# Kernel optimization log

Hardware: AMD Instinct MI355X
Metric: run time of the kernel (lower is better)

The kernel has to match this reference:

```python
import jax, jax.numpy as jnp
import numpy as np

DESIRED_SIZE = 512.0
STRIDE = DESIRED_SIZE / 16.0  # Constants.desired_size / 16
EPS = 1e-7
IOU_SCALE = 2.0
DIOU_SCALE = 0.5
SL1_SCALE = 1.0
GOOD_MULT = 2.0
BAD_MULT = 1.5


def setup_inputs() -> dict:
    key = jax.random.key(0)
    k1, k2 = jax.random.split(key)
    pred_boxes = jax.random.normal(k1, (64, 3, 32, 32, 5), dtype=jnp.float32)
    # uniform in [0, desired_size); every row has positive sum => all boxes valid,
    # so filter_and_trim keeps exactly max_boxes=100 per batch (fixed-k topk)
    target_boxes = jax.random.uniform(k2, (64, 100, 4), dtype=jnp.float32) * DESIRED_SIZE
    return {"pred_boxes": pred_boxes, "target_boxes": target_boxes}


def _postprocess(pred):
    # pred: [B, A, H, W, 5] -> absolute (x, y, w, h), conf
    B, A, H, W, _ = pred.shape
    cx = jnp.arange(W, dtype=pred.dtype)[None, None, None, :]
    cy = jnp.arange(H, dtype=pred.dtype)[None, None, :, None]
    x = (jax.nn.sigmoid(pred[..., 0]) + cx) * STRIDE
    y = (jax.nn.sigmoid(pred[..., 1]) + cy) * STRIDE
    wh = jnp.exp(pred[..., 2:4]) * STRIDE
    conf = jax.nn.sigmoid(pred[..., 4])
    return jnp.stack([x, y, wh[..., 0], wh[..., 1]], axis=-1), conf


def _fix_box_coordinates(b, epsilon=1.0):
    x1 = jnp.minimum(b[..., 0], b[..., 2])
    y1 = jnp.minimum(b[..., 1], b[..., 3])
    x2 = jnp.maximum(b[..., 0], b[..., 2])
    y2 = jnp.maximum(b[..., 1], b[..., 3])
    x2 = jnp.where(x1 == x2, x1 + epsilon, x2)
    y2 = jnp.where(y1 == y2, y1 + epsilon, y2)
    return jnp.stack([x1, y1, x2, y2], axis=-1)


def _yolo_to_corners(b):
    xc, yc, w, h = b[..., 0], b[..., 1], b[..., 2], b[..., 3]
    return jnp.stack([xc - w / 2, yc - h / 2, xc + w / 2, yc + h / 2], axis=-1)


def _box_iou(a, b):
    # torchvision.ops.box_iou: a [N,4], b [M,4] -> [N,M]
    area_a = (a[:, 2] - a[:, 0]) * (a[:, 3] - a[:, 1])
    area_b = (b[:, 2] - b[:, 0]) * (b[:, 3] - b[:, 1])
    lt = jnp.maximum(a[:, None, :2], b[None, :, :2])
    rb = jnp.minimum(a[:, None, 2:], b[None, :, 2:])
    wh = jnp.clip(rb - lt, 0.0)
    inter = wh[..., 0] * wh[..., 1]
    return inter / (area_a[:, None] + area_b[None, :] - inter)


def _diou_loss(p, t, eps=EPS):
    pa = jnp.clip(p[..., 2] - p[..., 0], 0.0) * jnp.clip(p[..., 3] - p[..., 1], 0.0)
    ta = jnp.clip(t[..., 2] - t[..., 0], 0.0) * jnp.clip(t[..., 3] - t[..., 1], 0.0)
    ix1 = jnp.maximum(p[..., 0], t[..., 0]); iy1 = jnp.maximum(p[..., 1], t[..., 1])
    ix2 = jnp.minimum(p[..., 2], t[..., 2]); iy2 = jnp.minimum(p[..., 3], t[..., 3])
    inter = jnp.clip(ix2 - ix1, 0.0) * jnp.clip(iy2 - iy1, 0.0)
    iou = inter / (pa + ta - inter + eps)
    pcx = (p[..., 0] + p[..., 2]) / 2; pcy = (p[..., 1] + p[..., 3]) / 2
    tcx = (t[..., 0] + t[..., 2]) / 2; tcy = (t[..., 1] + t[..., 3]) / 2
    cdist = (pcx - tcx) ** 2 + (pcy - tcy) ** 2
    ex1 = jnp.minimum(p[..., 0], t[..., 0]); ey1 = jnp.minimum(p[..., 1], t[..., 1])
    ex2 = jnp.maximum(p[..., 2], t[..., 2]); ey2 = jnp.maximum(p[..., 3], t[..., 3])
    diag = (ex2 - ex1) ** 2 + (ey2 - ey1) ** 2
    return 1.0 - (iou - cdist / (diag + eps))


def _smooth_l1_mean(p, t):
    d = p - t
    ad = jnp.abs(d)
    return jnp.mean(jnp.where(ad < 1.0, 0.5 * d * d, ad - 0.5))


def reference(pred_boxes, target_boxes):
    # negative-size penalty computed on RAW (pre-postprocess) width/height
    pw = pred_boxes[..., 2]
    ph = pred_boxes[..., 3]
    neg_pen = (jnp.clip(1.0 - pw, 0.0) + jnp.clip(1.0 - ph, 0.0)).mean()

    coords, conf = _postprocess(pred_boxes)
    B = pred_boxes.shape[0]
    coords = coords.reshape(B, -1, 4)   # [B, A*H*W, 4]
    conf = conf.reshape(B, -1)          # [B, A*H*W]

    K = target_boxes.shape[1]  # all targets valid by construction -> fixed k
    topv, topi = jax.lax.top_k(conf, K)                      # [B, K]
    pred_sel = jnp.take_along_axis(coords, topi[..., None], axis=1)  # [B, K, 4]

    target_flat = target_boxes.reshape(-1, 4)   # [N, 4], N = B*K
    pred_flat = pred_sel.reshape(-1, 4)
    conf_flat = topv.reshape(-1, 1)             # [N, 1]

    target_c = _fix_box_coordinates(target_flat)
    pred_c = _yolo_to_corners(pred_flat)

    # IoULoss: max over preds of full NxN IoU matrix, per target
    iou_mat = _box_iou(pred_c, target_c)
    max_iou = jnp.clip(jnp.nan_to_num(jnp.max(iou_mat, axis=0)), 0.0)
    iou_loss = 1.0 - max_iou                    # [N]

    sl1 = _smooth_l1_mean(pred_c, target_c) / DESIRED_SIZE  # scalar
    diou = _diou_loss(pred_c, target_c)         # [N]

    max_loss = IOU_SCALE + DIOU_SCALE + SL1_SCALE  # 3.5
    # NOTE: source adds UNSCALED diou into x (faithful to original)
    x = iou_loss * IOU_SCALE + diou + sl1 * SL1_SCALE   # [N]
    y = conf_flat                                        # [N, 1] -> broadcast to [N, N]
    good = jnp.sqrt((0.0 - x) ** 2 + (1.0 - y) ** 2) * GOOD_MULT
    bad = jnp.sqrt((max_loss - x) ** 2 + (1.0 - y) ** 2) * BAD_MULT
    losses = jnp.clip(jnp.mean(good - bad) + max_loss * BAD_MULT, 0.0)
    return losses + neg_pen
```

## Files before the change

### kernel.cpp

```cpp
#include <hip/hip_runtime.h>
#include <cmath>

#define NKEY 3072
#define KSEL 100
#define PCHUNK 200

static __device__ __forceinline__ float sigf(float v) {
    return 1.0f / (1.0f + expf(-v));
}

static __device__ double block_reduce_sum(double v) {
    __shared__ double sh[4];
    __syncthreads();
    for (int off = 32; off > 0; off >>= 1) v += __shfl_down(v, off, 64);
    int lane = threadIdx.x & 63, wid = threadIdx.x >> 6;
    if (lane == 0) sh[wid] = v;
    __syncthreads();
    v = (threadIdx.x < 4) ? sh[threadIdx.x] : 0.0;
    if (wid == 0) {
        v += __shfl_down(v, 2, 64);
        v += __shfl_down(v, 1, 64);
    }
    return v;
}

__global__ __launch_bounds__(256) void k_topk(const float* __restrict__ pred,
                                              const float* __restrict__ tgt,
                                              float* __restrict__ predc,
                                              float* __restrict__ targc,
                                              float* __restrict__ confv,
                                              unsigned int* __restrict__ maxiou_bits,
                                              double* __restrict__ negp ,
                                              float* __restrict__ diouv,
                                              double* __restrict__ sl1p ,
                                              double* __restrict__ pair_sum,
                                              unsigned int* __restrict__ done_cnt) {
    const int b = blockIdx.x;
    const int t = threadIdx.x;

    __shared__ unsigned long long keys[NKEY];
    __shared__ unsigned int hist[256];
    __shared__ unsigned long long sel[KSEL];
    __shared__ float4 pbox[KSEL];
    __shared__ float4 tbox[KSEL];
    __shared__ unsigned long long tkey_sh;
    __shared__ unsigned int scnt;
    __shared__ int bdigit_sh;
    __shared__ int bk_sh;

    if (b == 0 && t == 0) { *pair_sum = 0.0; *done_cnt = 0u; }

    if (t < KSEL) {
        int n = b * KSEL + t;
        const float* tb = tgt + (size_t)n * 4;
        float a0 = tb[0], a1 = tb[1], a2 = tb[2], a3 = tb[3];
        float x1 = fminf(a0, a2), y1 = fminf(a1, a3);
        float x2 = fmaxf(a0, a2), y2 = fmaxf(a1, a3);
        if (x1 == x2) x2 = x1 + 1.0f;
        if (y1 == y2) y2 = y1 + 1.0f;
        targc[n * 4 + 0] = x1; targc[n * 4 + 1] = y1;
        targc[n * 4 + 2] = x2; targc[n * 4 + 3] = y2;
        tbox[t] = make_float4(x1, y1, x2, y2);
        maxiou_bits[n] = 0u;
    }
    if (t == 0) scnt = 0;

    const float* pb = pred + (size_t)b * (NKEY * 5);
    float negacc = 0.0f;
    for (int r = 0; r < 12; ++r) {
        int idx = t + r * 256;
        const float* pe = pb + (size_t)idx * 5;
        float w = pe[2], h = pe[3], cl = pe[4];
        negacc += fmaxf(1.0f - w, 0.0f) + fmaxf(1.0f - h, 0.0f);
        float c = sigf(cl);
        keys[idx] = ((unsigned long long)__float_as_uint(c) << 32)
                  | (unsigned long long)(0xFFFFFFFFu - (unsigned)idx);
    }
    {
        double v = block_reduce_sum((double)negacc);
        if (t == 0) negp[b] = v;
    }
    __syncthreads();

    unsigned long long prefix = 0ull;
    int plen = 0;
    int k = KSEL;
    bool done = false;
    for (int round = 0; round < 8 && !done; ++round) {
        hist[t] = 0u;
        __syncthreads();
        int shift = 56 - 8 * round;
        for (int r = 0; r < 12; ++r) {
            unsigned long long key = keys[t + r * 256];
            if (plen == 0 || (key >> (64 - plen)) == (prefix >> (64 - plen))) {
                atomicAdd(&hist[(unsigned)((key >> shift) & 0xFFull)], 1u);
            }
        }
        __syncthreads();
        if (t < 64) {
            unsigned s0 = hist[4 * t + 0], s1 = hist[4 * t + 1];
            unsigned s2 = hist[4 * t + 2], s3 = hist[4 * t + 3];
            unsigned ssum = s0 + s1 + s2 + s3;
            unsigned suf = ssum;
            for (int off = 1; off < 64; off <<= 1) {
                unsigned o = __shfl_down(suf, off, 64);
                if (t + off < 64) suf += o;
            }
            unsigned above = suf - ssum;
            if (above < (unsigned)k && suf >= (unsigned)k) {
                unsigned hh[4] = {s0, s1, s2, s3};
                unsigned cum = above;
                for (int q = 3; q >= 0; --q) {
                    unsigned c = hh[q];
                    if (cum + c >= (unsigned)k) { bdigit_sh = 4 * t + q; bk_sh = k - (int)cum; break; }
                    cum += c;
                }
            }
        }
        __syncthreads();
        int d = bdigit_sh;
        k = bk_sh;
        prefix |= ((unsigned long long)(unsigned)d) << shift;
        plen += 8;
        unsigned ceq = hist[d];
        if (ceq == 1u) {
            for (int r = 0; r < 12; ++r) {
                unsigned long long key = keys[t + r * 256];
                if ((key >> (64 - plen)) == (prefix >> (64 - plen))) tkey_sh = key;
            }
            done = true;
        }
        __syncthreads();
    }
    unsigned long long T = tkey_sh;

    for (int r = 0; r < 12; ++r) {
        unsigned long long key = keys[t + r * 256];
        if (key >= T) {
            unsigned pos = atomicAdd(&scnt, 1u);
            sel[pos] = key;
        }
    }
    __syncthreads();
    if (t < KSEL) {
        unsigned long long key = sel[t];
        int rank = 0;
        for (int p = 0; p < KSEL; ++p) rank += (sel[p] > key) ? 1 : 0;
        unsigned idx = 0xFFFFFFFFu - (unsigned)(key & 0xFFFFFFFFull);
        float conf = __uint_as_float((unsigned)(key >> 32));
        int n = b * KSEL + rank;
        confv[n] = conf;
        const float* pe = pb + (size_t)idx * 5;
        int w = idx & 31, h = (idx >> 5) & 31;
        float x  = (sigf(pe[0]) + (float)w) * 32.0f;
        float y  = (sigf(pe[1]) + (float)h) * 32.0f;
        float bw = expf(pe[2]) * 32.0f;
        float bh = expf(pe[3]) * 32.0f;
        float4 pc = make_float4(x - bw * 0.5f, y - bh * 0.5f,
                                x + bw * 0.5f, y + bh * 0.5f);
        predc[n * 4 + 0] = pc.x; predc[n * 4 + 1] = pc.y;
        predc[n * 4 + 2] = pc.z; predc[n * 4 + 3] = pc.w;
        pbox[rank] = pc;
    }
    __syncthreads();

    double s = 0.0;
    if (t < KSEL) {
        float4 p = pbox[t];
        float4 tj = tbox[t];
        float pa = fmaxf(p.z - p.x, 0.f) * fmaxf(p.w - p.y, 0.f);
        float ta2 = fmaxf(tj.z - tj.x, 0.f) * fmaxf(tj.w - tj.y, 0.f);
        float ix1 = fmaxf(p.x, tj.x), iy1 = fmaxf(p.y, tj.y);
        float ix2 = fminf(p.z, tj.z), iy2 = fminf(p.w, tj.w);
        float inter = fmaxf(ix2 - ix1, 0.f) * fmaxf(iy2 - iy1, 0.f);
        float iou = inter / (pa + ta2 - inter + 1e-7f);
        float pcx = (p.x + p.z) * 0.5f, pcy = (p.y + p.w) * 0.5f;
        float tcx = (tj.x + tj.z) * 0.5f, tcy = (tj.y + tj.w) * 0.5f;
        float cd = (pcx - tcx) * (pcx - tcx) + (pcy - tcy) * (pcy - tcy);
        float ex1 = fminf(p.x, tj.x), ey1 = fminf(p.y, tj.y);
        float ex2 = fmaxf(p.z, tj.z), ey2 = fmaxf(p.w, tj.w);
        float dg = (ex2 - ex1) * (ex2 - ex1) + (ey2 - ey1) * (ey2 - ey1);
        diouv[b * KSEL + t] = 1.0f - (iou - cd / (dg + 1e-7f));
        float d0 = p.x - tj.x, d1 = p.y - tj.y, d2 = p.z - tj.z, d3 = p.w - tj.w;
        float a0 = fabsf(d0), a1 = fabsf(d1), a2 = fabsf(d2), a3 = fabsf(d3);
        s += (double)(a0 < 1.f ? 0.5f * d0 * d0 : a0 - 0.5f);
        s += (double)(a1 < 1.f ? 0.5f * d1 * d1 : a1 - 0.5f);
        s += (double)(a2 < 1.f ? 0.5f * d2 * d2 : a2 - 0.5f);
        s += (double)(a3 < 1.f ? 0.5f * d3 * d3 : a3 - 0.5f);
    }
    double v = block_reduce_sum(s);
    if (t == 0) sl1p[b] = v;
}

__global__ __launch_bounds__(256) void k_maxiou(const float* __restrict__ predc,
                                                const float* __restrict__ targc,
                                                unsigned int* __restrict__ maxiou_bits) {
    __shared__ float4 pl[PCHUNK];
    __shared__ float pa_sh[PCHUNK];
    int t = threadIdx.x;
    int j = blockIdx.x * 256 + t;
    const float4* pc4 = (const float4*)predc;
    int i0 = blockIdx.y * PCHUNK;
    for (int i = t; i < PCHUNK; i += 256) {
        float4 p = pc4[i0 + i];
        pl[i] = p;
        pa_sh[i] = (p.z - p.x) * (p.w - p.y);
    }
    float4 tj = ((const float4*)targc)[j];
    float ta = (tj.z - tj.x) * (tj.w - tj.y);
    __syncthreads();
    float m0 = 0.0f, m1 = 0.0f;
    #pragma unroll 2
    for (int i = 0; i < PCHUNK; i += 2) {
        float4 p = pl[i];
        float w0 = fmaxf(fminf(p.z, tj.z) - fmaxf(p.x, tj.x), 0.0f);
        float h0 = fmaxf(fminf(p.w, tj.w) - fmaxf(p.y, tj.y), 0.0f);
        float in0 = w0 * h0;
        float iou0 = in0 * __builtin_amdgcn_rcpf(pa_sh[i] + ta - in0);
        m0 = fmaxf(m0, iou0);
        float4 q = pl[i + 1];
        float w1 = fmaxf(fminf(q.z, tj.z) - fmaxf(q.x, tj.x), 0.0f);
        float h1 = fmaxf(fminf(q.w, tj.w) - fmaxf(q.y, tj.y), 0.0f);
        float in1 = w1 * h1;
        float iou1 = in1 * __builtin_amdgcn_rcpf(pa_sh[i + 1] + ta - in1);
        m1 = fmaxf(m1, iou1);
    }
    m0 = fmaxf(m0, m1);
    atomicMax(&maxiou_bits[j], __float_as_uint(m0));
}

__global__ __launch_bounds__(256) void k_pair(const unsigned int* __restrict__ maxiou_bits,
                                              const float* __restrict__ diouv,
                                              const float* __restrict__ confv,
                                              const double* __restrict__ sl1p ,
                                              const double* __restrict__ negp,
                                              double* __restrict__ pair_sum,
                                              unsigned int* __restrict__ done_cnt,
                                              float* __restrict__ out) {
    __shared__ float oy2s[256];
    __shared__ float sl1_sh;
    int t = threadIdx.x;
    int j = blockIdx.x * 256 + t;
    if (t == 0) {
        double s = 0.0;
        for (int i = 0; i < 64; ++i) s += sl1p[i];
        sl1_sh = (float)(s / 25600.0 / 512.0);
    }
    {
        float oy = 1.0f - confv[blockIdx.y * 256 + t];
        oy2s[t] = oy * oy;
    }
    float mj = __uint_as_float(maxiou_bits[j]);
    float dj = diouv[j];
    __syncthreads();
    float xj = (1.0f - mj) * 2.0f + dj + sl1_sh;
    float a2 = xj * xj;
    float bb = 3.5f - xj;
    float b2 = bb * bb;
    float acc0 = 0.0f, acc1 = 0.0f;
    #pragma unroll 4
    for (int i = 0; i < 256; i += 2) {
        float o0 = oy2s[i], o1 = oy2s[i + 1];
        acc0 += 2.0f * __builtin_amdgcn_sqrtf(a2 + o0)
              - 1.5f * __builtin_amdgcn_sqrtf(b2 + o0);
        acc1 += 2.0f * __builtin_amdgcn_sqrtf(a2 + o1)
              - 1.5f * __builtin_amdgcn_sqrtf(b2 + o1);
    }
    double v = block_reduce_sum((double)(acc0 + acc1));
    if (t == 0) {
        atomicAdd(pair_sum, v);
        __threadfence();
        unsigned prev = atomicAdd(done_cnt, 1u);
        if (prev == 624u) {
            double ps = atomicAdd(pair_sum, 0.0);
            double ns = 0.0;
            for (int i = 0; i < 64; ++i) ns += negp[i];
            double mean_pair = ps / 40960000.0;
            float losses = fmaxf((float)mean_pair + 5.25f, 0.0f);
            float neg = (float)(ns / 196608.0);
            out[0] = losses + neg;
        }
    }
}


extern "C" void kernel_launch(void* const* d_in, const int* in_sizes, int n_in,
                              void* d_out, int out_size, void* d_ws, size_t ws_size,
                              hipStream_t stream) {
    const float* pred = (const float*)d_in[0];
    const float* tgt  = (const float*)d_in[1];
    float* out = (float*)d_out;

    char* ws = (char*)d_ws;
    double* negp     = (double*)ws;
    double* sl1p     = negp + 64;
    double* pair_sum = negp + 128;
    unsigned int* done_cnt = (unsigned int*)(negp + 129);
    float* fbase  = (float*)(ws + 6400);
    float* predc  = fbase;
    float* targc  = fbase + 25600;
    float* confv  = fbase + 51200;
    float* diouv  = fbase + 57600;
    unsigned int* maxiou_bits = (unsigned int*)(fbase + 64000);

    k_topk<<<64, 256, 0, stream>>>(pred, tgt, predc, targc, confv, maxiou_bits,
                                   negp, diouv, sl1p, pair_sum, done_cnt);
    k_maxiou<<<dim3(25, 32), 256, 0, stream>>>(predc, targc, maxiou_bits);
    k_pair<<<dim3(25, 25), 256, 0, stream>>>(maxiou_bits, diouv, confv, sl1p,
                                             negp, pair_sum, done_cnt, out);
}
```

Measured before the change: 115.8 us.

## Fuse three kernels into one persistent kernel with grid-wide barriers

```diff
diff --git a/kernel.cpp b/kernel.cpp
--- a/kernel.cpp
+++ b/kernel.cpp
@@ -4,6 +4,7 @@
 #define NKEY 3072
 #define KSEL 100
 #define PCHUNK 200
+#define NBLK 256
 
 static __device__ __forceinline__ float sigf(float v) {
     return 1.0f / (1.0f + expf(-v));
@@ -24,18 +25,26 @@
     return v;
 }
 
-__global__ __launch_bounds__(256) void k_topk(const float* __restrict__ pred,
-                                              const float* __restrict__ tgt,
-                                              float* __restrict__ predc,
-                                              float* __restrict__ targc,
-                                              float* __restrict__ confv,
-                                              unsigned int* __restrict__ maxiou_bits,
-                                              double* __restrict__ negp ,
-                                              float* __restrict__ diouv,
-                                              double* __restrict__ sl1p ,
-                                              double* __restrict__ pair_sum,
-                                              unsigned int* __restrict__ done_cnt) {
-    const int b = blockIdx.x;
+static __device__ void gsync(unsigned int* bar, unsigned int target) {
+    __syncthreads();
+    if (threadIdx.x == 0) {
+        __threadfence();
+        atomicAdd(bar, 1u);
+        while (atomicAdd(bar, 0u) < target) __builtin_amdgcn_s_sleep(8);
+        __threadfence();
+    }
+    __syncthreads();
+}
+
+__global__ __launch_bounds__(256) void k_fused(
+        const float* __restrict__ pred, const float* __restrict__ tgt,
+        float* __restrict__ predc, float* __restrict__ targc,
+        float* __restrict__ confv, unsigned int* __restrict__ maxiou_bits,
+        double* __restrict__ negp , float* __restrict__ diouv,
+        double* __restrict__ sl1p , unsigned int* __restrict__ bar,
+        double* __restrict__ pair_sum, unsigned int* __restrict__ done_cnt,
+        float* __restrict__ out) {
+    const int bid = blockIdx.x;
     const int t = threadIdx.x;
 
     __shared__ unsigned long long keys[NKEY];
@@ -47,231 +56,236 @@
     __shared__ unsigned int scnt;
     __shared__ int bdigit_sh;
     __shared__ int bk_sh;
-
-    if (b == 0 && t == 0) { *pair_sum = 0.0; *done_cnt = 0u; }
-
-    if (t < KSEL) {
-        int n = b * KSEL + t;
-        const float* tb = tgt + (size_t)n * 4;
-        float a0 = tb[0], a1 = tb[1], a2 = tb[2], a3 = tb[3];
-        float x1 = fminf(a0, a2), y1 = fminf(a1, a3);
-        float x2 = fmaxf(a0, a2), y2 = fmaxf(a1, a3);
-        if (x1 == x2) x2 = x1 + 1.0f;
-        if (y1 == y2) y2 = y1 + 1.0f;
-        targc[n * 4 + 0] = x1; targc[n * 4 + 1] = y1;
-        targc[n * 4 + 2] = x2; targc[n * 4 + 3] = y2;
-        tbox[t] = make_float4(x1, y1, x2, y2);
-        maxiou_bits[n] = 0u;
-    }
-    if (t == 0) scnt = 0;
-
-    const float* pb = pred + (size_t)b * (NKEY * 5);
-    float negacc = 0.0f;
-    for (int r = 0; r < 12; ++r) {
-        int idx = t + r * 256;
-        const float* pe = pb + (size_t)idx * 5;
-        float w = pe[2], h = pe[3], cl = pe[4];
-        negacc += fmaxf(1.0f - w, 0.0f) + fmaxf(1.0f - h, 0.0f);
-        float c = sigf(cl);
-        keys[idx] = ((unsigned long long)__float_as_uint(c) << 32)
-                  | (unsigned long long)(0xFFFFFFFFu - (unsigned)idx);
-    }
-    {
-        double v = block_reduce_sum((double)negacc);
-        if (t == 0) negp[b] = v;
-    }
-    __syncthreads();
-
-    unsigned long long prefix = 0ull;
-    int plen = 0;
-    int k = KSEL;
-    bool done = false;
-    for (int round = 0; round < 8 && !done; ++round) {
-        hist[t] = 0u;
-        __syncthreads();
-        int shift = 56 - 8 * round;
+    __shared__ float4 pl[PCHUNK];
+    __shared__ float pa_sh[PCHUNK];
+    __shared__ float oy2s[256];
+    __shared__ float sl1_sh;
+
+    if (bid < 64) {
+        const int b = bid;
+
+        if (t < KSEL) {
+            int n = b * KSEL + t;
+            const float* tb = tgt + (size_t)n * 4;
+            float a0 = tb[0], a1 = tb[1], a2 = tb[2], a3 = tb[3];
+            float x1 = fminf(a0, a2), y1 = fminf(a1, a3);
+            float x2 = fmaxf(a0, a2), y2 = fmaxf(a1, a3);
+            if (x1 == x2) x2 = x1 + 1.0f;
+            if (y1 == y2) y2 = y1 + 1.0f;
+            targc[n * 4 + 0] = x1; targc[n * 4 + 1] = y1;
+            targc[n * 4 + 2] = x2; targc[n * 4 + 3] = y2;
+            tbox[t] = make_float4(x1, y1, x2, y2);
+            maxiou_bits[n] = 0u;
+        }
+        if (t == 0) scnt = 0;
+
+        const float* pb = pred + (size_t)b * (NKEY * 5);
+        float negacc = 0.0f;
+        for (int r = 0; r < 12; ++r) {
+            int idx = t + r * 256;
+            const float* pe = pb + (size_t)idx * 5;
+            float w = pe[2], h = pe[3], cl = pe[4];
+            negacc += fmaxf(1.0f - w, 0.0f) + fmaxf(1.0f - h, 0.0f);
+            float c = sigf(cl);
+            keys[idx] = ((unsigned long long)__float_as_uint(c) << 32)
+                      | (unsigned long long)(0xFFFFFFFFu - (unsigned)idx);
+        }
+        {
+            double v = block_reduce_sum((double)negacc);
+            if (t == 0) negp[b] = v;
+        }
+        __syncthreads();
+
+        unsigned long long prefix = 0ull;
+        int plen = 0;
+        int k = KSEL;
+        bool done = false;
+        for (int round = 0; round < 8 && !done; ++round) {
+            hist[t] = 0u;
+            __syncthreads();
+            int shift = 56 - 8 * round;
+            for (int r = 0; r < 12; ++r) {
+                unsigned long long key = keys[t + r * 256];
+                if (plen == 0 || (key >> (64 - plen)) == (prefix >> (64 - plen))) {
+                    atomicAdd(&hist[(unsigned)((key >> shift) & 0xFFull)], 1u);
+                }
+            }
+            __syncthreads();
+            if (t < 64) {
+                unsigned s0 = hist[4 * t + 0], s1 = hist[4 * t + 1];
+                unsigned s2 = hist[4 * t + 2], s3 = hist[4 * t + 3];
+                unsigned ssum = s0 + s1 + s2 + s3;
+                unsigned suf = ssum;
+                for (int off = 1; off < 64; off <<= 1) {
+                    unsigned o = __shfl_down(suf, off, 64);
+                    if (t + off < 64) suf += o;
+                }
+                unsigned above = suf - ssum;
+                if (above < (unsigned)k && suf >= (unsigned)k) {
+                    unsigned hh[4] = {s0, s1, s2, s3};
+                    unsigned cum = above;
+                    for (int q = 3; q >= 0; --q) {
+                        unsigned c = hh[q];
+                        if (cum + c >= (unsigned)k) { bdigit_sh = 4 * t + q; bk_sh = k - (int)cum; break; }
+                        cum += c;
+                    }
+                }
+            }
+            __syncthreads();
+            int d = bdigit_sh;
+            k = bk_sh;
+            prefix |= ((unsigned long long)(unsigned)d) << shift;
+            plen += 8;
+            unsigned ceq = hist[d];
+            if (ceq == 1u) {
+                for (int r = 0; r < 12; ++r) {
+                    unsigned long long key = keys[t + r * 256];
+                    if ((key >> (64 - plen)) == (prefix >> (64 - plen))) tkey_sh = key;
+                }
+                done = true;
+            }
+            __syncthreads();
+        }
+        unsigned long long T = tkey_sh;
+
         for (int r = 0; r < 12; ++r) {
             unsigned long long key = keys[t + r * 256];
-            if (plen == 0 || (key >> (64 - plen)) == (prefix >> (64 - plen))) {
-                atomicAdd(&hist[(unsigned)((key >> shift) & 0xFFull)], 1u);
+            if (key >= T) {
+                unsigned pos = atomicAdd(&scnt, 1u);
+                sel[pos] = key;
             }
         }
         __syncthreads();
-        if (t < 64) {
-            unsigned s0 = hist[4 * t + 0], s1 = hist[4 * t + 1];
-            unsigned s2 = hist[4 * t + 2], s3 = hist[4 * t + 3];
-            unsigned ssum = s0 + s1 + s2 + s3;
-            unsigned suf = ssum;
-            for (int off = 1; off < 64; off <<= 1) {
-                unsigned o = __shfl_down(suf, off, 64);
-                if (t + off < 64) suf += o;
-            }
-            unsigned above = suf - ssum;
-            if (above < (unsigned)k && suf >= (unsigned)k) {
-                unsigned hh[4] = {s0, s1, s2, s3};
-                unsigned cum = above;
-                for (int q = 3; q >= 0; --q) {
-                    unsigned c = hh[q];
-                    if (cum + c >= (unsigned)k) { bdigit_sh = 4 * t + q; bk_sh = k - (int)cum; break; }
-                    cum += c;
-                }
-            }
-        }
-        __syncthreads();
-        int d = bdigit_sh;
-        k = bk_sh;
-        prefix |= ((unsigned long long)(unsigned)d) << shift;
-        plen += 8;
-        unsigned ceq = hist[d];
-        if (ceq == 1u) {
-            for (int r = 0; r < 12; ++r) {
-                unsigned long long key = keys[t + r * 256];
-                if ((key >> (64 - plen)) == (prefix >> (64 - plen))) tkey_sh = key;
-            }
-            done = true;
-        }
-        __syncthreads();
-    }
-    unsigned long long T = tkey_sh;
-
-    for (int r = 0; r < 12; ++r) {
-        unsigned long long key = keys[t + r * 256];
-        if (key >= T) {
-            unsigned pos = atomicAdd(&scnt, 1u);
-            sel[pos] = key;
-        }
-    }
-    __syncthreads();
-    if (t < KSEL) {
-        unsigned long long key = sel[t];
-        int rank = 0;
-        for (int p = 0; p < KSEL; ++p) rank += (sel[p] > key) ? 1 : 0;
-        unsigned idx = 0xFFFFFFFFu - (unsigned)(key & 0xFFFFFFFFull);
-        float conf = __uint_as_float((unsigned)(key >> 32));
-        int n = b * KSEL + rank;
-        confv[n] = conf;
-        const float* pe = pb + (size_t)idx * 5;
-        int w = idx & 31, h = (idx >> 5) & 31;
-        float x  = (sigf(pe[0]) + (float)w) * 32.0f;
-        float y  = (sigf(pe[1]) + (float)h) * 32.0f;
-        float bw = expf(pe[2]) * 32.0f;
-        float bh = expf(pe[3]) * 32.0f;
-        float4 pc = make_float4(x - bw * 0.5f, y - bh * 0.5f,
-                                x + bw * 0.5f, y + bh * 0.5f);
-        predc[n * 4 + 0] = pc.x; predc[n * 4 + 1] = pc.y;
-        predc[n * 4 + 2] = pc.z; predc[n * 4 + 3] = pc.w;
-        pbox[rank] = pc;
-    }
-    __syncthreads();
-
-    double s = 0.0;
-    if (t < KSEL) {
-        float4 p = pbox[t];
-        float4 tj = tbox[t];
-        float pa = fmaxf(p.z - p.x, 0.f) * fmaxf(p.w - p.y, 0.f);
-        float ta2 = fmaxf(tj.z - tj.x, 0.f) * fmaxf(tj.w - tj.y, 0.f);
-        float ix1 = fmaxf(p.x, tj.x), iy1 = fmaxf(p.y, tj.y);
-        float ix2 = fminf(p.z, tj.z), iy2 = fminf(p.w, tj.w);
-        float inter = fmaxf(ix2 - ix1, 0.f) * fmaxf(iy2 - iy1, 0.f);
-        float iou = inter / (pa + ta2 - inter + 1e-7f);
-        float pcx = (p.x + p.z) * 0.5f, pcy = (p.y + p.w) * 0.5f;
-        float tcx = (tj.x + tj.z) * 0.5f, tcy = (tj.y + tj.w) * 0.5f;
-        float cd = (pcx - tcx) * (pcx - tcx) + (pcy - tcy) * (pcy - tcy);
-        float ex1 = fminf(p.x, tj.x), ey1 = fminf(p.y, tj.y);
-        float ex2 = fmaxf(p.z, tj.z), ey2 = fmaxf(p.w, tj.w);
-        float dg = (ex2 - ex1) * (ex2 - ex1) + (ey2 - ey1) * (ey2 - ey1);
-        diouv[b * KSEL + t] = 1.0f - (iou - cd / (dg + 1e-7f));
-        float d0 = p.x - tj.x, d1 = p.y - tj.y, d2 = p.z - tj.z, d3 = p.w - tj.w;
-        float a0 = fabsf(d0), a1 = fabsf(d1), a2 = fabsf(d2), a3 = fabsf(d3);
-        s += (double)(a0 < 1.f ? 0.5f * d0 * d0 : a0 - 0.5f);
-        s += (double)(a1 < 1.f ? 0.5f * d1 * d1 : a1 - 0.5f);
-        s += (double)(a2 < 1.f ? 0.5f * d2 * d2 : a2 - 0.5f);
-        s += (double)(a3 < 1.f ? 0.5f * d3 * d3 : a3 - 0.5f);
-    }
-    double v = block_reduce_sum(s);
-    if (t == 0) sl1p[b] = v;
-}
-
-__global__ __launch_bounds__(256) void k_maxiou(const float* __restrict__ predc,
-                                                const float* __restrict__ targc,
-                                                unsigned int* __restrict__ maxiou_bits) {
-    __shared__ float4 pl[PCHUNK];
-    __shared__ float pa_sh[PCHUNK];
-    int t = threadIdx.x;
-    int j = blockIdx.x * 256 + t;
+        if (t < KSEL) {
+            unsigned long long key = sel[t];
+            int rank = 0;
+            for (int p = 0; p < KSEL; ++p) rank += (sel[p] > key) ? 1 : 0;
+            unsigned idx = 0xFFFFFFFFu - (unsigned)(key & 0xFFFFFFFFull);
+            float conf = __uint_as_float((unsigned)(key >> 32));
+            int n = b * KSEL + rank;
+            confv[n] = conf;
+            const float* pe = pb + (size_t)idx * 5;
+            int w = idx & 31, h = (idx >> 5) & 31;
+            float x  = (sigf(pe[0]) + (float)w) * 32.0f;
+            float y  = (sigf(pe[1]) + (float)h) * 32.0f;
+            float bw = expf(pe[2]) * 32.0f;
+            float bh = expf(pe[3]) * 32.0f;
+            float4 pc = make_float4(x - bw * 0.5f, y - bh * 0.5f,
+                                    x + bw * 0.5f, y + bh * 0.5f);
+            predc[n * 4 + 0] = pc.x; predc[n * 4 + 1] = pc.y;
+            predc[n * 4 + 2] = pc.z; predc[n * 4 + 3] = pc.w;
+            pbox[rank] = pc;
+        }
+        __syncthreads();
+
+        double s = 0.0;
+        if (t < KSEL) {
+            float4 p = pbox[t];
+            float4 tj = tbox[t];
+            float pa = fmaxf(p.z - p.x, 0.f) * fmaxf(p.w - p.y, 0.f);
+            float ta2 = fmaxf(tj.z - tj.x, 0.f) * fmaxf(tj.w - tj.y, 0.f);
+            float ix1 = fmaxf(p.x, tj.x), iy1 = fmaxf(p.y, tj.y);
+            float ix2 = fminf(p.z, tj.z), iy2 = fminf(p.w, tj.w);
+            float inter = fmaxf(ix2 - ix1, 0.f) * fmaxf(iy2 - iy1, 0.f);
+            float iou = inter / (pa + ta2 - inter + 1e-7f);
+            float pcx = (p.x + p.z) * 0.5f, pcy = (p.y + p.w) * 0.5f;
+            float tcx = (tj.x + tj.z) * 0.5f, tcy = (tj.y + tj.w) * 0.5f;
+            float cd = (pcx - tcx) * (pcx - tcx) + (pcy - tcy) * (pcy - tcy);
+            float ex1 = fminf(p.x, tj.x), ey1 = fminf(p.y, tj.y);
+            float ex2 = fmaxf(p.z, tj.z), ey2 = fmaxf(p.w, tj.w);
+            float dg = (ex2 - ex1) * (ex2 - ex1) + (ey2 - ey1) * (ey2 - ey1);
+            diouv[b * KSEL + t] = 1.0f - (iou - cd / (dg + 1e-7f));
+            float d0 = p.x - tj.x, d1 = p.y - tj.y, d2 = p.z - tj.z, d3 = p.w - tj.w;
+            float a0 = fabsf(d0), a1 = fabsf(d1), a2 = fabsf(d2), a3 = fabsf(d3);
+            s += (double)(a0 < 1.f ? 0.5f * d0 * d0 : a0 - 0.5f);
+            s += (double)(a1 < 1.f ? 0.5f * d1 * d1 : a1 - 0.5f);
+            s += (double)(a2 < 1.f ? 0.5f * d2 * d2 : a2 - 0.5f);
+            s += (double)(a3 < 1.f ? 0.5f * d3 * d3 : a3 - 0.5f);
+        }
+        double v = block_reduce_sum(s);
+        if (t == 0) sl1p[b] = v;
+    }
+
+    gsync(bar, NBLK);
+
     const float4* pc4 = (const float4*)predc;
-    int i0 = blockIdx.y * PCHUNK;
-    for (int i = t; i < PCHUNK; i += 256) {
-        float4 p = pc4[i0 + i];
-        pl[i] = p;
-        pa_sh[i] = (p.z - p.x) * (p.w - p.y);
-    }
-    float4 tj = ((const float4*)targc)[j];
-    float ta = (tj.z - tj.x) * (tj.w - tj.y);
-    __syncthreads();
-    float m0 = 0.0f, m1 = 0.0f;
-    #pragma unroll 2
-    for (int i = 0; i < PCHUNK; i += 2) {
-        float4 p = pl[i];
-        float w0 = fmaxf(fminf(p.z, tj.z) - fmaxf(p.x, tj.x), 0.0f);
-        float h0 = fmaxf(fminf(p.w, tj.w) - fmaxf(p.y, tj.y), 0.0f);
-        float in0 = w0 * h0;
-        float iou0 = in0 * __builtin_amdgcn_rcpf(pa_sh[i] + ta - in0);
-        m0 = fmaxf(m0, iou0);
-        float4 q = pl[i + 1];
-        float w1 = fmaxf(fminf(q.z, tj.z) - fmaxf(q.x, tj.x), 0.0f);
-        float h1 = fmaxf(fminf(q.w, tj.w) - fmaxf(q.y, tj.y), 0.0f);
-        float in1 = w1 * h1;
-        float iou1 = in1 * __builtin_amdgcn_rcpf(pa_sh[i + 1] + ta - in1);
-        m1 = fmaxf(m1, iou1);
-    }
-    m0 = fmaxf(m0, m1);
-    atomicMax(&maxiou_bits[j], __float_as_uint(m0));
-}
-
-__global__ __launch_bounds__(256) void k_pair(const unsigned int* __restrict__ maxiou_bits,
-                                              const float* __restrict__ diouv,
-                                              const float* __restrict__ confv,
-                                              const double* __restrict__ sl1p ,
-                                              const double* __restrict__ negp,
-                                              double* __restrict__ pair_sum,
-                                              unsigned int* __restrict__ done_cnt,
-                                              float* __restrict__ out) {
-    __shared__ float oy2s[256];
-    __shared__ float sl1_sh;
-    int t = threadIdx.x;
-    int j = blockIdx.x * 256 + t;
+    const float4* tc4 = (const float4*)targc;
+    for (int tile = bid; tile < 800; tile += NBLK) {
+        int tx = tile >> 5;
+        int ty = tile & 31;
+        int j = tx * 256 + t;
+        int i0 = ty * PCHUNK;
+        if (t < PCHUNK) {
+            float4 p = pc4[i0 + t];
+            pl[t] = p;
+            pa_sh[t] = (p.z - p.x) * (p.w - p.y);
+        }
+        float4 tj = tc4[j];
+        float ta = (tj.z - tj.x) * (tj.w - tj.y);
+        __syncthreads();
+        float m0 = 0.0f, m1 = 0.0f;
+        #pragma unroll 2
+        for (int i = 0; i < PCHUNK; i += 2) {
+            float4 p = pl[i];
+            float w0 = fmaxf(fminf(p.z, tj.z) - fmaxf(p.x, tj.x), 0.0f);
+            float h0 = fmaxf(fminf(p.w, tj.w) - fmaxf(p.y, tj.y), 0.0f);
+            float in0 = w0 * h0;
+            float iou0 = in0 * __builtin_amdgcn_rcpf(pa_sh[i] + ta - in0);
+            m0 = fmaxf(m0, iou0);
+            float4 q = pl[i + 1];
+            float w1 = fmaxf(fminf(q.z, tj.z) - fmaxf(q.x, tj.x), 0.0f);
+            float h1 = fmaxf(fminf(q.w, tj.w) - fmaxf(q.y, tj.y), 0.0f);
+            float in1 = w1 * h1;
+            float iou1 = in1 * __builtin_amdgcn_rcpf(pa_sh[i + 1] + ta - in1);
+            m1 = fmaxf(m1, iou1);
+        }
+        m0 = fmaxf(m0, m1);
+        atomicMax(&maxiou_bits[j], __float_as_uint(m0));
+        __syncthreads();
+    }
+
+    gsync(bar, 2 * NBLK);
+
     if (t == 0) {
         double s = 0.0;
         for (int i = 0; i < 64; ++i) s += sl1p[i];
         sl1_sh = (float)(s / 25600.0 / 512.0);
     }
-    {
-        float oy = 1.0f - confv[blockIdx.y * 256 + t];
-        oy2s[t] = oy * oy;
-    }
-    float mj = __uint_as_float(maxiou_bits[j]);
-    float dj = diouv[j];
-    __syncthreads();
-    float xj = (1.0f - mj) * 2.0f + dj + sl1_sh;
-    float a2 = xj * xj;
-    float bb = 3.5f - xj;
-    float b2 = bb * bb;
-    float acc0 = 0.0f, acc1 = 0.0f;
-    #pragma unroll 4
-    for (int i = 0; i < 256; i += 2) {
-        float o0 = oy2s[i], o1 = oy2s[i + 1];
-        acc0 += 2.0f * __builtin_amdgcn_sqrtf(a2 + o0)
-              - 1.5f * __builtin_amdgcn_sqrtf(b2 + o0);
-        acc1 += 2.0f * __builtin_amdgcn_sqrtf(a2 + o1)
-              - 1.5f * __builtin_amdgcn_sqrtf(b2 + o1);
-    }
-    double v = block_reduce_sum((double)(acc0 + acc1));
+    double accd = 0.0;
+    for (int tile = bid; tile < 625; tile += NBLK) {
+        int tx = tile / 25;
+        int ty = tile - tx * 25;
+        {
+            float oy = 1.0f - confv[ty * 256 + t];
+            oy2s[t] = oy * oy;
+        }
+        int j = tx * 256 + t;
+        float mj = __uint_as_float(maxiou_bits[j]);
+        float dj = diouv[j];
+        __syncthreads();
+        float xj = (1.0f - mj) * 2.0f + dj + sl1_sh;
+        float a2 = xj * xj;
+        float bb = 3.5f - xj;
+        float b2 = bb * bb;
+        float acc0 = 0.0f, acc1 = 0.0f;
+        #pragma unroll 4
+        for (int i = 0; i < 256; i += 2) {
+            float o0 = oy2s[i], o1 = oy2s[i + 1];
+            acc0 += 2.0f * __builtin_amdgcn_sqrtf(a2 + o0)
+                  - 1.5f * __builtin_amdgcn_sqrtf(b2 + o0);
+            acc1 += 2.0f * __builtin_amdgcn_sqrtf(a2 + o1)
+                  - 1.5f * __builtin_amdgcn_sqrtf(b2 + o1);
+        }
+        accd += (double)(acc0 + acc1);
+        __syncthreads();
+    }
+    double v = block_reduce_sum(accd);
     if (t == 0) {
         atomicAdd(pair_sum, v);
         __threadfence();
         unsigned prev = atomicAdd(done_cnt, 1u);
-        if (prev == 624u) {
+        if (prev == NBLK - 1u) {
+            __threadfence();
             double ps = atomicAdd(pair_sum, 0.0);
             double ns = 0.0;
             for (int i = 0; i < 64; ++i) ns += negp[i];
@@ -292,10 +306,11 @@
     float* out = (float*)d_out;
 
     char* ws = (char*)d_ws;
-    double* negp     = (double*)ws;
-    double* sl1p     = negp + 64;
-    double* pair_sum = negp + 128;
-    unsigned int* done_cnt = (unsigned int*)(negp + 129);
+    unsigned int* bar      = (unsigned int*)(ws + 0);
+    double* pair_sum       = (double*)(ws + 8);
+    unsigned int* done_cnt = (unsigned int*)(ws + 16);
+    double* negp  = (double*)(ws + 64);
+    double* sl1p  = (double*)(ws + 576);
     float* fbase  = (float*)(ws + 6400);
     float* predc  = fbase;
     float* targc  = fbase + 25600;
@@ -303,9 +318,7 @@
     float* diouv  = fbase + 57600;
     unsigned int* maxiou_bits = (unsigned int*)(fbase + 64000);
 
-    k_topk<<<64, 256, 0, stream>>>(pred, tgt, predc, targc, confv, maxiou_bits,
-                                   negp, diouv, sl1p, pair_sum, done_cnt);
-    k_maxiou<<<dim3(25, 32), 256, 0, stream>>>(predc, targc, maxiou_bits);
-    k_pair<<<dim3(25, 25), 256, 0, stream>>>(maxiou_bits, diouv, confv, sl1p,
-                                             negp, pair_sum, done_cnt, out);
-}
+    hipMemsetAsync(ws, 0, 64, stream);
+    k_fused<<<NBLK, 256, 0, stream>>>(pred, tgt, predc, targc, confv, maxiou_bits,
+                                      negp, diouv, sl1p, bar, pair_sum, done_cnt, out);
+}
```

Result: slower. 151.0 us (+30.4%).
